# Optimization experiments

Measured on AMD Instinct MI355X. Metric: run time of the kernel, lower is better.

Reference implementation:

```python
import jax, jax.numpy as jnp
import numpy as np

B, CIN, COUT, H, W = 8, 256, 256, 64, 64


def setup_inputs() -> dict:
    key = jax.random.key(0)
    k1, k2, k3 = jax.random.split(key, 3)
    x = jax.random.normal(k1, (B, CIN, H, W), dtype=jnp.float32)
    style = jax.random.normal(k2, (B, CIN), dtype=jnp.float32)
    # kaiming_normal_ (fan_in = CIN*3*3, gain = sqrt(2))
    fan_in = CIN * 9
    weight = jax.random.normal(k3, (COUT, CIN, 3, 3), dtype=jnp.float32) * np.sqrt(2.0 / fan_in)
    return {"x": x, "style": style, "weight": weight}


def reference(x, style, weight):
    b, cin, h, w = x.shape
    cout = weight.shape[0]
    # modulate: [B, Cout, Cin, 3, 3]
    mw = style[:, None, :, None, None] * weight[None]
    # demodulate
    sigma = jnp.sqrt(jnp.sum(mw * mw, axis=(2, 3, 4), keepdims=True) + 1e-8)
    dw = mw / sigma
    # per-sample conv via grouped convolution (groups = B)
    x_g = x.reshape(1, b * cin, h, w)
    w_g = dw.reshape(b * cout, cin, 3, 3)
    out = jax.lax.conv_general_dilated(
        x_g, w_g,
        window_strides=(1, 1),
        padding=((1, 1), (1, 1)),
        feature_group_count=b,
        dimension_numbers=("NCHW", "OIHW", "NCHW"),
    )
    return out.reshape(b, cout, h, w)
```

## Files before the change

### kernel.cpp

```cpp
#include <hip/hip_runtime.h>

#define B_ 8
#define CIN_ 256
#define COUT_ 256

typedef short short8_t __attribute__((ext_vector_type(8)));
typedef float float4_t __attribute__((ext_vector_type(4)));

#define DWA_SHORTS   (B_ * 9 * 32 * COUT_ * 8)
#define XPRE_SHORTS  (B_ * 8 * 66 * 66 * 32)

__device__ __forceinline__ unsigned short f2bf(float f) {
    union { float f; unsigned u; } v; v.f = f;
    unsigned u = v.u;
    unsigned r = (u + 0x7fffu + ((u >> 16) & 1u)) >> 16;
    return (unsigned short)r;
}

__global__ __launch_bounds__(256) void k_xpre(const float* __restrict__ x,
                                              unsigned short* __restrict__ xpre) {
    const int h_out = blockIdx.x;
    const int cb = blockIdx.y, b = blockIdx.z;
    const int t = threadIdx.x;
    const int h_in = h_out - 1;
    unsigned short* dst_row = xpre + (((size_t)(b * 8 + cb) * 66 + h_out)) * 66 * 32;
#pragma unroll
    for (int pass = 0; pass < 2; ++pass) {
        int p = t + pass * 256;
        if (p >= 264) break;
        int w_out = p >> 2, g = p & 3;
        int w_in = w_out - 1;
        short8_t v = (short8_t){0, 0, 0, 0, 0, 0, 0, 0};
        if ((unsigned)h_in < 64u && (unsigned)w_in < 64u) {
            const float* xp = x + (((size_t)(b * CIN_ + cb * 32 + g * 8)) * 64 + h_in) * 64 + w_in;
#pragma unroll
            for (int j = 0; j < 8; ++j) v[j] = (short)f2bf(xp[(size_t)j * 4096]);
        }
        *(short8_t*)(dst_row + (size_t)w_out * 32 + g * 8) = v;
    }
}

__global__ __launch_bounds__(256) void k_modulate(const float* __restrict__ weight,
                                                  const float* __restrict__ style,
                                                  unsigned short* __restrict__ dwA) {
    __shared__ float wlds[4 * 2304];
    const int t = threadIdx.x;
    const int co0 = blockIdx.x * 4;
    const int co_l = t >> 6;
    const int lane = t & 63;
    const int co = co0 + co_l;

    const float* wp = weight + (size_t)co0 * 2304;
#pragma unroll
    for (int k = 0; k < 36; ++k) wlds[t + 256 * k] = wp[t + 256 * k];
    __syncthreads();

    float wv[4][9];
    float ss[4];
#pragma unroll
    for (int k = 0; k < 4; ++k) {
        float a = 0.f;
#pragma unroll
        for (int tap = 0; tap < 9; ++tap) {
            float w = wlds[co_l * 2304 + (lane + 64 * k) * 9 + tap];
            wv[k][tap] = w;
            a += w * w;
        }
        ss[k] = a;
    }
    float sv[8][4];
#pragma unroll
    for (int b = 0; b < 8; ++b)
#pragma unroll
        for (int k = 0; k < 4; ++k) sv[b][k] = style[b * CIN_ + lane + 64 * k];

    float inv[8];
#pragma unroll
    for (int b = 0; b < 8; ++b) {
        float part = 0.f;
#pragma unroll
        for (int k = 0; k < 4; ++k) part += sv[b][k] * sv[b][k] * ss[k];
#pragma unroll
        for (int off = 32; off > 0; off >>= 1) part += __shfl_xor(part, off, 64);
        inv[b] = 1.0f / sqrtf(part + 1e-8f);
    }

    const size_t base = (size_t)co * 8 + (lane & 7) + (size_t)(lane >> 3) * 2048;
#pragma unroll
    for (int b = 0; b < 8; ++b)
#pragma unroll
        for (int tap = 0; tap < 9; ++tap)
#pragma unroll
            for (int k = 0; k < 4; ++k) {
                size_t addr = ((size_t)(b * 9 + tap) * 32 + k * 8) * 2048 + base;
                dwA[addr] = f2bf(wv[k][tap] * sv[b][k] * inv[b]);
            }
}

__global__ __launch_bounds__(256) void k_conv(const unsigned short* __restrict__ xpre,
                                              const unsigned short* __restrict__ dwA,
                                              float* __restrict__ out) {
    __shared__ __align__(16) unsigned short xs[2][4 * 66 * 40];

    const int rowgrp = blockIdx.x;
    const int co_tile = blockIdx.y;
    const int b = blockIdx.z;
    const int tid = threadIdx.x;
    const int lane = tid & 63, wid = tid >> 6;
    const int wave_m = wid >> 1, wave_n = wid & 1;
    const int quad = lane >> 4, l16 = lane & 15;
    const int r0 = rowgrp * 2;
    const int co_base = co_tile * 128 + wave_m * 64;

    float4_t acc[4][4];
#pragma unroll
    for (int mi = 0; mi < 4; ++mi)
#pragma unroll
        for (int ni = 0; ni < 4; ++ni) acc[mi][ni] = (float4_t){0.f, 0.f, 0.f, 0.f};

    short8_t st[5];
    auto load_regs = [&](int cb) {
        const unsigned short* s = xpre + ((size_t)((b * 8 + cb) * 66 + r0)) * 2112;
#pragma unroll
        for (int it = 0; it < 4; ++it)
            st[it] = *(const short8_t*)(s + (size_t)(tid + it * 256) * 8);
        if (tid < 32) st[4] = *(const short8_t*)(s + (size_t)(tid + 1024) * 8);
    };
    auto store_lds = [&](int buf) {
        unsigned short* d = xs[buf];
#pragma unroll
        for (int it = 0; it < 4; ++it) {
            int c = tid + it * 256;
            *(short8_t*)(d + (c >> 2) * 40 + (c & 3) * 8) = st[it];
        }
        if (tid < 32) {
            int c = tid + 1024;
            *(short8_t*)(d + (c >> 2) * 40 + (c & 3) * 8) = st[4];
        }
    };

    short8_t abuf[3][4];
    auto loadA = [&](short8_t* dst, int acb, int atap) {
        const unsigned short* Ab = dwA + ((size_t)(b * 9 + atap) * 32 + acb * 4 + quad) * 2048;
#pragma unroll
        for (int mi = 0; mi < 4; ++mi)
            dst[mi] = *(const short8_t*)(Ab + (co_base + mi * 16 + l16) * 8);
    };

    load_regs(0);
    loadA(abuf[0], 0, 0);
    loadA(abuf[1], 0, 1);

    for (int cb = 0; cb < 8; ++cb) {
        store_lds(cb & 1);
        __syncthreads();
        if (cb < 7) load_regs(cb + 1);

        const unsigned short* xb = xs[cb & 1];
#pragma unroll
        for (int tap = 0; tap < 9; ++tap) {
            const int nl = tap + 2;
            const int acb = cb + nl / 9, atap = nl % 9;
            if (acb < 8) loadA(abuf[nl % 3], acb, atap);

            const int dh = tap / 3, dwc = tap % 3;
            const unsigned short* brow = xb + (wave_n + dh) * 66 * 40;
            short8_t bf[4];
#pragma unroll
            for (int ni = 0; ni < 4; ++ni)
                bf[ni] = *(const short8_t*)(brow + (ni * 16 + l16 + dwc) * 40 + quad * 8);

            const short8_t* ac = abuf[tap % 3];
#pragma unroll
            for (int mi = 0; mi < 4; ++mi)
#pragma unroll
                for (int ni = 0; ni < 4; ++ni)
                    acc[mi][ni] = __builtin_amdgcn_mfma_f32_16x16x32_bf16(
                        ac[mi], bf[ni], acc[mi][ni], 0, 0, 0);
        }
    }

    const int orow = r0 + wave_n;
#pragma unroll
    for (int mi = 0; mi < 4; ++mi)
#pragma unroll
        for (int ni = 0; ni < 4; ++ni)
#pragma unroll
            for (int r = 0; r < 4; ++r) {
                int co = co_base + mi * 16 + quad * 4 + r;
                int c = ni * 16 + l16;
                out[(((size_t)b * COUT_ + co) * 64 + orow) * 64 + c] = acc[mi][ni][r];
            }
}

extern "C" void kernel_launch(void* const* d_in, const int* in_sizes, int n_in,
                              void* d_out, int out_size, void* d_ws, size_t ws_size,
                              hipStream_t stream) {
    const float* x = (const float*)d_in[0];
    const float* style = (const float*)d_in[1];
    const float* weight = (const float*)d_in[2];
    float* out = (float*)d_out;

    unsigned short* dwA = (unsigned short*)d_ws;
    unsigned short* xpre = dwA + DWA_SHORTS;

    k_xpre<<<dim3(66, 8, B_), 256, 0, stream>>>(x, xpre);
    k_modulate<<<dim3(64), 256, 0, stream>>>(weight, style, dwA);
    k_conv<<<dim3(32, 2, B_), 256, 0, stream>>>(xpre, dwA, out);
}
```

Baseline: 141.8 us.

## Switch conv to 32x32x16 MFMA with one row per block, merge prep kernels

Merges the input-pack and weight-modulate kernels into one launch, saving a kernel launch. The conv kernel now uses 32x32x16 bf16 MFMA instead of 16x16x32, with a 128 co by 64 px tile per block covering one output row (64x2x8 blocks). The LDS tile is smaller and unpadded and the A buffer is double rather than triple buffered, so register and LDS pressure drop and occupancy can rise (launch bounds 4). In exchange, each block reads a 3-row halo for one output row instead of 4 rows for two, and the unpadded LDS layout may cause bank conflicts.

Measured after the change: 153.5 us. 8.2% more time.

```diff
diff --git a/kernel.cpp b/kernel.cpp
--- a/kernel.cpp
+++ b/kernel.cpp
@@ -5,7 +5,7 @@
 #define COUT_ 256
 
 typedef short short8_t __attribute__((ext_vector_type(8)));
-typedef float float4_t __attribute__((ext_vector_type(4)));
+typedef float float16_t __attribute__((ext_vector_type(16)));
 
 #define DWA_SHORTS   (B_ * 9 * 32 * COUT_ * 8)
 #define XPRE_SHORTS  (B_ * 8 * 66 * 66 * 32)
@@ -17,139 +17,148 @@
     return (unsigned short)r;
 }
 
-__global__ __launch_bounds__(256) void k_xpre(const float* __restrict__ x,
-                                              unsigned short* __restrict__ xpre) {
-    const int h_out = blockIdx.x;
-    const int cb = blockIdx.y, b = blockIdx.z;
+__global__ __launch_bounds__(256) void k_prep(const float* __restrict__ x,
+                                              const float* __restrict__ style,
+                                              const float* __restrict__ weight,
+                                              unsigned short* __restrict__ xpre,
+                                              unsigned short* __restrict__ dwA) {
+    __shared__ float wlds[4 * 2304];
+    const int bid = blockIdx.x;
     const int t = threadIdx.x;
-    const int h_in = h_out - 1;
-    unsigned short* dst_row = xpre + (((size_t)(b * 8 + cb) * 66 + h_out)) * 66 * 32;
-#pragma unroll
-    for (int pass = 0; pass < 2; ++pass) {
-        int p = t + pass * 256;
-        if (p >= 264) break;
-        int w_out = p >> 2, g = p & 3;
-        int w_in = w_out - 1;
-        short8_t v = (short8_t){0, 0, 0, 0, 0, 0, 0, 0};
-        if ((unsigned)h_in < 64u && (unsigned)w_in < 64u) {
-            const float* xp = x + (((size_t)(b * CIN_ + cb * 32 + g * 8)) * 64 + h_in) * 64 + w_in;
-#pragma unroll
-            for (int j = 0; j < 8; ++j) v[j] = (short)f2bf(xp[(size_t)j * 4096]);
-        }
-        *(short8_t*)(dst_row + (size_t)w_out * 32 + g * 8) = v;
+
+    if (bid < 4224) {
+        const int h_out = bid % 66;
+        const int t2 = bid / 66;
+        const int cb = t2 & 7, b = t2 >> 3;
+        const int h_in = h_out - 1;
+        unsigned short* dst_row = xpre + ((size_t)(b * 8 + cb) * 66 + h_out) * 66 * 32;
+#pragma unroll
+        for (int pass = 0; pass < 2; ++pass) {
+            int p = t + pass * 256;
+            if (p >= 264) break;
+            int w_out = p >> 2, g = p & 3;
+            int w_in = w_out - 1;
+            short8_t v = (short8_t){0, 0, 0, 0, 0, 0, 0, 0};
+            if ((unsigned)h_in < 64u && (unsigned)w_in < 64u) {
+                const float* xp =
+                    x + (((size_t)(b * CIN_ + cb * 32 + g * 8)) * 64 + h_in) * 64 + w_in;
+#pragma unroll
+                for (int j = 0; j < 8; ++j) v[j] = (short)f2bf(xp[(size_t)j * 4096]);
+            }
+            *(short8_t*)(dst_row + (size_t)w_out * 32 + g * 8) = v;
+        }
+    } else {
+        const int co0 = (bid - 4224) * 4;
+        const int co_l = t >> 6;
+        const int lane = t & 63;
+        const int co = co0 + co_l;
+
+        const float* wp = weight + (size_t)co0 * 2304;
+#pragma unroll
+        for (int k = 0; k < 36; ++k) wlds[t + 256 * k] = wp[t + 256 * k];
+        __syncthreads();
+
+        float wv[4][9];
+        float ss[4];
+#pragma unroll
+        for (int k = 0; k < 4; ++k) {
+            float a = 0.f;
+#pragma unroll
+            for (int tap = 0; tap < 9; ++tap) {
+                float w = wlds[co_l * 2304 + (lane + 64 * k) * 9 + tap];
+                wv[k][tap] = w;
+                a += w * w;
+            }
+            ss[k] = a;
+        }
+        float sv[8][4];
+#pragma unroll
+        for (int b = 0; b < 8; ++b)
+#pragma unroll
+            for (int k = 0; k < 4; ++k) sv[b][k] = style[b * CIN_ + lane + 64 * k];
+
+        float inv[8];
+#pragma unroll
+        for (int b = 0; b < 8; ++b) {
+            float part = 0.f;
+#pragma unroll
+            for (int k = 0; k < 4; ++k) part += sv[b][k] * sv[b][k] * ss[k];
+#pragma unroll
+            for (int off = 32; off > 0; off >>= 1) part += __shfl_xor(part, off, 64);
+            inv[b] = 1.0f / sqrtf(part + 1e-8f);
+        }
+
+        const size_t base = (size_t)co * 8 + (lane & 7) + (size_t)(lane >> 3) * 2048;
+#pragma unroll
+        for (int b = 0; b < 8; ++b)
+#pragma unroll
+            for (int tap = 0; tap < 9; ++tap)
+#pragma unroll
+                for (int k = 0; k < 4; ++k) {
+                    size_t addr = ((size_t)(b * 9 + tap) * 32 + k * 8) * 2048 + base;
+                    dwA[addr] = f2bf(wv[k][tap] * sv[b][k] * inv[b]);
+                }
     }
 }
 
-__global__ __launch_bounds__(256) void k_modulate(const float* __restrict__ weight,
-                                                  const float* __restrict__ style,
-                                                  unsigned short* __restrict__ dwA) {
-    __shared__ float wlds[4 * 2304];
-    const int t = threadIdx.x;
-    const int co0 = blockIdx.x * 4;
-    const int co_l = t >> 6;
-    const int lane = t & 63;
-    const int co = co0 + co_l;
-
-    const float* wp = weight + (size_t)co0 * 2304;
-#pragma unroll
-    for (int k = 0; k < 36; ++k) wlds[t + 256 * k] = wp[t + 256 * k];
-    __syncthreads();
-
-    float wv[4][9];
-    float ss[4];
-#pragma unroll
-    for (int k = 0; k < 4; ++k) {
-        float a = 0.f;
-#pragma unroll
-        for (int tap = 0; tap < 9; ++tap) {
-            float w = wlds[co_l * 2304 + (lane + 64 * k) * 9 + tap];
-            wv[k][tap] = w;
-            a += w * w;
-        }
-        ss[k] = a;
-    }
-    float sv[8][4];
-#pragma unroll
-    for (int b = 0; b < 8; ++b)
-#pragma unroll
-        for (int k = 0; k < 4; ++k) sv[b][k] = style[b * CIN_ + lane + 64 * k];
-
-    float inv[8];
-#pragma unroll
-    for (int b = 0; b < 8; ++b) {
-        float part = 0.f;
-#pragma unroll
-        for (int k = 0; k < 4; ++k) part += sv[b][k] * sv[b][k] * ss[k];
-#pragma unroll
-        for (int off = 32; off > 0; off >>= 1) part += __shfl_xor(part, off, 64);
-        inv[b] = 1.0f / sqrtf(part + 1e-8f);
-    }
-
-    const size_t base = (size_t)co * 8 + (lane & 7) + (size_t)(lane >> 3) * 2048;
-#pragma unroll
-    for (int b = 0; b < 8; ++b)
-#pragma unroll
-        for (int tap = 0; tap < 9; ++tap)
-#pragma unroll
-            for (int k = 0; k < 4; ++k) {
-                size_t addr = ((size_t)(b * 9 + tap) * 32 + k * 8) * 2048 + base;
-                dwA[addr] = f2bf(wv[k][tap] * sv[b][k] * inv[b]);
-            }
-}
-
-__global__ __launch_bounds__(256) void k_conv(const unsigned short* __restrict__ xpre,
-                                              const unsigned short* __restrict__ dwA,
-                                              float* __restrict__ out) {
-    __shared__ __align__(16) unsigned short xs[2][4 * 66 * 40];
-
-    const int rowgrp = blockIdx.x;
+__global__ __launch_bounds__(256, 4) void k_conv(const unsigned short* __restrict__ xpre,
+                                                 const unsigned short* __restrict__ dwA,
+                                                 float* __restrict__ out) {
+    __shared__ __align__(16) unsigned short xs[2][12 * 66 * 8];
+
+    const int row = blockIdx.x;
     const int co_tile = blockIdx.y;
     const int b = blockIdx.z;
     const int tid = threadIdx.x;
     const int lane = tid & 63, wid = tid >> 6;
     const int wave_m = wid >> 1, wave_n = wid & 1;
-    const int quad = lane >> 4, l16 = lane & 15;
-    const int r0 = rowgrp * 2;
+    const int l32 = lane & 31, kh = lane >> 5;
     const int co_base = co_tile * 128 + wave_m * 64;
 
-    float4_t acc[4][4];
-#pragma unroll
-    for (int mi = 0; mi < 4; ++mi)
-#pragma unroll
-        for (int ni = 0; ni < 4; ++ni) acc[mi][ni] = (float4_t){0.f, 0.f, 0.f, 0.f};
-
-    short8_t st[5];
+    float16_t acc[2];
+#pragma unroll
+    for (int mi = 0; mi < 2; ++mi)
+#pragma unroll
+        for (int r = 0; r < 16; ++r) acc[mi][r] = 0.f;
+
+    short8_t st[4];
     auto load_regs = [&](int cb) {
-        const unsigned short* s = xpre + ((size_t)((b * 8 + cb) * 66 + r0)) * 2112;
-#pragma unroll
-        for (int it = 0; it < 4; ++it)
-            st[it] = *(const short8_t*)(s + (size_t)(tid + it * 256) * 8);
-        if (tid < 32) st[4] = *(const short8_t*)(s + (size_t)(tid + 1024) * 8);
+        const unsigned short* s = xpre + (((size_t)(b * 8 + cb) * 66 + row)) * (66 * 32);
+#pragma unroll
+        for (int it = 0; it < 3; ++it) {
+            int c = tid + it * 256;
+            int rowg = c / 66;
+            int col = c - rowg * 66;
+            st[it] = *(const short8_t*)(s + (size_t)((rowg >> 2) * 2112 + col * 32 + (rowg & 3) * 8));
+        }
+        if (tid < 24) {
+            int c = tid + 768;
+            int rowg = c / 66;
+            int col = c - rowg * 66;
+            st[3] = *(const short8_t*)(s + (size_t)((rowg >> 2) * 2112 + col * 32 + (rowg & 3) * 8));
+        }
     };
     auto store_lds = [&](int buf) {
         unsigned short* d = xs[buf];
 #pragma unroll
-        for (int it = 0; it < 4; ++it) {
-            int c = tid + it * 256;
-            *(short8_t*)(d + (c >> 2) * 40 + (c & 3) * 8) = st[it];
-        }
-        if (tid < 32) {
-            int c = tid + 1024;
-            *(short8_t*)(d + (c >> 2) * 40 + (c & 3) * 8) = st[4];
-        }
+        for (int it = 0; it < 3; ++it)
+            *(short8_t*)(d + (size_t)(tid + it * 256) * 8) = st[it];
+        if (tid < 24) *(short8_t*)(d + (size_t)(tid + 768) * 8) = st[3];
     };
 
-    short8_t abuf[3][4];
+    short8_t abuf[2][4];
     auto loadA = [&](short8_t* dst, int acb, int atap) {
-        const unsigned short* Ab = dwA + ((size_t)(b * 9 + atap) * 32 + acb * 4 + quad) * 2048;
-#pragma unroll
-        for (int mi = 0; mi < 4; ++mi)
-            dst[mi] = *(const short8_t*)(Ab + (co_base + mi * 16 + l16) * 8);
+        const unsigned short* base = dwA + ((size_t)(b * 9 + atap) * 32 + acb * 4 + kh) * 2048;
+#pragma unroll
+        for (int mi = 0; mi < 2; ++mi)
+#pragma unroll
+            for (int ks = 0; ks < 2; ++ks)
+                dst[mi * 2 + ks] =
+                    *(const short8_t*)(base + (size_t)ks * 4096 + (co_base + mi * 32 + l32) * 8);
     };
 
     load_regs(0);
     loadA(abuf[0], 0, 0);
-    loadA(abuf[1], 0, 1);
 
     for (int cb = 0; cb < 8; ++cb) {
         store_lds(cb & 1);
@@ -159,38 +168,37 @@
         const unsigned short* xb = xs[cb & 1];
 #pragma unroll
         for (int tap = 0; tap < 9; ++tap) {
-            const int nl = tap + 2;
+            const int par = (cb + tap) & 1;
+            const int nl = tap + 1;
             const int acb = cb + nl / 9, atap = nl % 9;
-            if (acb < 8) loadA(abuf[nl % 3], acb, atap);
-
-            const int dh = tap / 3, dwc = tap % 3;
-            const unsigned short* brow = xb + (wave_n + dh) * 66 * 40;
-            short8_t bf[4];
-#pragma unroll
-            for (int ni = 0; ni < 4; ++ni)
-                bf[ni] = *(const short8_t*)(brow + (ni * 16 + l16 + dwc) * 40 + quad * 8);
-
-            const short8_t* ac = abuf[tap % 3];
-#pragma unroll
-            for (int mi = 0; mi < 4; ++mi)
-#pragma unroll
-                for (int ni = 0; ni < 4; ++ni)
-                    acc[mi][ni] = __builtin_amdgcn_mfma_f32_16x16x32_bf16(
-                        ac[mi], bf[ni], acc[mi][ni], 0, 0, 0);
+            if (acb < 8) loadA(abuf[par ^ 1], acb, atap);
+
+            const int dh = tap / 3, dwc = tap - dh * 3;
+            const int col = wave_n * 32 + l32 + dwc;
+            short8_t bf[2];
+#pragma unroll
+            for (int ks = 0; ks < 2; ++ks) {
+                int g = ks * 2 + kh;
+                bf[ks] = *(const short8_t*)(xb + (size_t)((dh * 4 + g) * 66 + col) * 8);
+            }
+            const short8_t* ac = abuf[par];
+#pragma unroll
+            for (int ks = 0; ks < 2; ++ks)
+#pragma unroll
+                for (int mi = 0; mi < 2; ++mi)
+                    acc[mi] = __builtin_amdgcn_mfma_f32_32x32x16_bf16(ac[mi * 2 + ks], bf[ks],
+                                                                      acc[mi], 0, 0, 0);
         }
     }
 
-    const int orow = r0 + wave_n;
-#pragma unroll
-    for (int mi = 0; mi < 4; ++mi)
-#pragma unroll
-        for (int ni = 0; ni < 4; ++ni)
-#pragma unroll
-            for (int r = 0; r < 4; ++r) {
-                int co = co_base + mi * 16 + quad * 4 + r;
-                int c = ni * 16 + l16;
-                out[(((size_t)b * COUT_ + co) * 64 + orow) * 64 + c] = acc[mi][ni][r];
-            }
+    const int colb = wave_n * 32 + l32;
+#pragma unroll
+    for (int mi = 0; mi < 2; ++mi)
+#pragma unroll
+        for (int r = 0; r < 16; ++r) {
+            int co = co_base + mi * 32 + (r & 3) + 8 * (r >> 2) + 4 * kh;
+            out[(((size_t)b * COUT_ + co) * 64 + row) * 64 + colb] = acc[mi][r];
+        }
 }
 
 extern "C" void kernel_launch(void* const* d_in, const int* in_sizes, int n_in,
@@ -204,7 +212,6 @@
     unsigned short* dwA = (unsigned short*)d_ws;
     unsigned short* xpre = dwA + DWA_SHORTS;
 
-    k_xpre<<<dim3(66, 8, B_), 256, 0, stream>>>(x, xpre);
-    k_modulate<<<dim3(64), 256, 0, stream>>>(weight, style, dwA);
-    k_conv<<<dim3(32, 2, B_), 256, 0, stream>>>(xpre, dwA, out);
-}
+    k_prep<<<dim3(4288), 256, 0, stream>>>(x, style, weight, xpre, dwA);
+    k_conv<<<dim3(64, 2, B_), 256, 0, stream>>>(xpre, dwA, out);
+}
```
